# Kernel tuning notes

Measured on AMD Instinct MI355X. Metric: run time of the kernel, lower is better.

The kernel has to match this reference:

```python
import jax, jax.numpy as jnp
import numpy as np

OUT_H = OUT_W = 7
SCALE = 1.0 / 16.0
E = 256
HEADS = 8
DH = E // HEADS
ROI_GRID = 14          # scaled roi side (fixed by construction -> static shapes)
N_ROIS = 512
FH, FW = 152, 256
NQ = OUT_H * OUT_W     # 49 content queries
S = ROI_GRID * ROI_GRID  # 196 keys per roi


def setup_inputs() -> dict:
    key = jax.random.key(0)
    ks = jax.random.split(key, 8)
    features = jax.random.normal(ks[0], (1, E, FH, FW), jnp.float32)
    # rois [N,5] = (batch_idx, x1, y1, x2, y2) in image coords; side 224 px so
    # the rounded scaled grid is exactly 14x14 for every roi.
    side = ROI_GRID / SCALE  # 224.0
    x1 = jax.random.uniform(ks[1], (N_ROIS,), minval=0.0, maxval=FW / SCALE - side)
    y1 = jax.random.uniform(ks[2], (N_ROIS,), minval=0.0, maxval=FH / SCALE - side)
    rois = jnp.stack([jnp.zeros(N_ROIS), x1, y1, x1 + side, y1 + side], axis=1)
    content_queries = jax.random.normal(ks[3], (NQ, E), jnp.float32) * 0.02
    in_proj_weight = jax.random.normal(ks[4], (3 * E, E), jnp.float32) / np.sqrt(E)
    in_proj_bias = jnp.zeros((3 * E,), jnp.float32)
    out_proj_weight = jax.random.normal(ks[5], (E, E), jnp.float32) / np.sqrt(E)
    out_proj_bias = jnp.zeros((E,), jnp.float32)
    balance_param = jnp.asarray(0.0, jnp.float32)  # hardsigmoid -> 0.5
    return dict(features=features, rois=rois, content_queries=content_queries,
                in_proj_weight=in_proj_weight, in_proj_bias=in_proj_bias,
                out_proj_weight=out_proj_weight, out_proj_bias=out_proj_bias,
                balance_param=balance_param)


def _bilinear(fmap, y, x):
    """torchvision roi_align bilinear sampling. fmap [C,H,W]; y,x flat [S]."""
    C, H, W = fmap.shape
    valid = ((y >= -1.0) & (y <= H) & (x >= -1.0) & (x <= W)).astype(fmap.dtype)
    y = jnp.clip(y, 0.0, H - 1.0)
    x = jnp.clip(x, 0.0, W - 1.0)
    y0 = jnp.floor(y); x0 = jnp.floor(x)
    y0i = y0.astype(jnp.int32); x0i = x0.astype(jnp.int32)
    y1i = jnp.minimum(y0i + 1, H - 1); x1i = jnp.minimum(x0i + 1, W - 1)
    ly = y - y0; lx = x - x0; hy = 1.0 - ly; hx = 1.0 - lx
    f = lambda yi, xi: fmap[:, yi, xi]  # [C, S]
    val = (hy * hx) * f(y0i, x0i) + (hy * lx) * f(y0i, x1i) \
        + (ly * hx) * f(y1i, x0i) + (ly * lx) * f(y1i, x1i)
    return val * valid


def _roi_align(fmap, roi4, out_h, out_w, scale, sr):
    """aligned=True RoIAlign for one roi, static sampling ratio sr."""
    x1, y1, x2, y2 = roi4
    sx = x1 * scale - 0.5
    sy = y1 * scale - 0.5
    bw = (x2 - x1) * scale / out_w
    bh = (y2 - y1) * scale / out_h
    offs = (jnp.arange(sr, dtype=fmap.dtype) + 0.5) / sr
    ys = sy + (jnp.arange(out_h, dtype=fmap.dtype)[:, None] + offs[None, :]) * bh  # [out_h,sr]
    xs = sx + (jnp.arange(out_w, dtype=fmap.dtype)[:, None] + offs[None, :]) * bw  # [out_w,sr]
    Y = jnp.broadcast_to(ys[:, :, None, None], (out_h, sr, out_w, sr)).reshape(-1)
    X = jnp.broadcast_to(xs[None, None, :, :], (out_h, sr, out_w, sr)).reshape(-1)
    vals = _bilinear(fmap, Y, X)  # [C, out_h*sr*out_w*sr]
    C = fmap.shape[0]
    return vals.reshape(C, out_h, sr, out_w, sr).mean(axis=(2, 4))  # [C,out_h,out_w]


def reference(features, rois, content_queries, in_proj_weight, in_proj_bias,
              out_proj_weight, out_proj_bias, balance_param):
    fmap = features[0]                       # single image batch
    roi4 = rois[:, 1:]                       # boxes in image coords
    balance = jnp.clip(balance_param / 6.0 + 0.5, 0.0, 1.0)  # hardsigmoid(_balance)

    # position pool: RoIAlign(7x7, spatial_scale, sampling_ratio=-1 -> 2, aligned)
    pos = jax.vmap(lambda r: _roi_align(fmap, r, OUT_H, OUT_W, SCALE, 2))(roi4)
    pos = pos * balance                      # [N, C, 7, 7]

    # per-roi content pool on scaled rois at scale 1.0, grid 14x14, sr=1
    sroi = roi4 * SCALE
    cf = jax.vmap(lambda r: _roi_align(fmap, r, ROI_GRID, ROI_GRID, 1.0, 1))(sroi)
    cf = cf.reshape(N_ROIS, E, S).transpose(0, 2, 1)  # [N, S, E] (flatten(2).permute)

    # nn.MultiheadAttention(E, HEADS): shared queries, per-roi keys/values
    Wq, Wk, Wv = jnp.split(in_proj_weight, 3, axis=0)
    bq, bk, bv = jnp.split(in_proj_bias, 3, axis=0)
    q = (content_queries @ Wq.T + bq).reshape(NQ, HEADS, DH).transpose(1, 0, 2)  # [h,Q,d]
    k = (cf @ Wk.T + bk).reshape(N_ROIS, S, HEADS, DH)
    v = (cf @ Wv.T + bv).reshape(N_ROIS, S, HEADS, DH)
    logits = jnp.einsum('hqd,nshd->nhqs', q, k) / np.sqrt(DH).astype(np.float32)
    attn = jax.nn.softmax(logits, axis=-1)                     # [N,h,Q,S]
    o = jnp.einsum('nhqs,nshd->nqhd', attn, v).reshape(N_ROIS, NQ, E)
    o = o @ out_proj_weight.T + out_proj_bias                  # [N, Q, E]
    att = o.transpose(0, 2, 1).reshape(N_ROIS, E, OUT_H, OUT_W)  # .T.reshape per roi

    return pos + att * (1.0 - balance)
```

## Files before the change

kernel.cpp:

```cpp
#include <hip/hip_runtime.h>
#include <stdint.h>

#define E_DIM 256
#define HEADS 8
#define NQ 49
#define S_TOT 196
#define NROIS 512
#define FH 152
#define FW 256
#define HW_TOT (FH*FW)

typedef unsigned short u16;
typedef short bf16x8 __attribute__((ext_vector_type(8)));
typedef float f32x4 __attribute__((ext_vector_type(4)));
typedef unsigned short us8 __attribute__((ext_vector_type(8)));

#define MFMA(a,b,c) __builtin_amdgcn_mfma_f32_16x16x32_bf16((a),(b),(c),0,0,0)

__device__ __forceinline__ u16 f2bf(float f) {
  union { float f; uint32_t u; } v; v.f = f;
  uint32_t u = v.u;
  return (u16)((u + 0x7FFFu + ((u >> 16) & 1u)) >> 16);
}
__device__ __forceinline__ float bf2f(u16 h) {
  union { uint32_t u; float f; } v; v.u = ((uint32_t)h) << 16;
  return v.f;
}
__device__ __forceinline__ uint32_t cvtpk(float lo, float hi) {
  uint32_t r;
  asm("v_cvt_pk_bf16_f32 %0, %1, %2" : "=v"(r) : "v"(lo), "v"(hi));
  return r;
}
__device__ __forceinline__ bf16x8 ld_frag(const u16* p) {
  union { uint2 d[2]; bf16x8 v; } t;
  t.d[0] = *(const uint2*)(p);
  t.d[1] = *(const uint2*)(p + 4);
  return t.v;
}
__device__ __forceinline__ bf16x8 ld_frag_g(const u16* p) {
  union { uint4 d; bf16x8 v; } t;
  t.d = *(const uint4*)(p);
  return t.v;
}
__device__ __forceinline__ void gll16(const u16* g, u16* l) {
  __builtin_amdgcn_global_load_lds(
      (__attribute__((address_space(1))) void*)(g),
      (__attribute__((address_space(3))) void*)(l), 16, 0, 0);
}
__device__ __forceinline__ void win_stencil(const u16* win, int p00, int hf,
                                            float w00, float w01, float w10, float w11,
                                            float o[16]) {
  const int cA = ((hf << 1)*225) << 3;
  const int cB = cA + (225 << 3);
  const int q0 = p00 << 3;
  us8 a00 = *(const us8*)(win + cA + q0);
  us8 a01 = *(const us8*)(win + cA + q0 + 8);
  us8 a10 = *(const us8*)(win + cA + q0 + 120);
  us8 a11 = *(const us8*)(win + cA + q0 + 128);
  us8 b00 = *(const us8*)(win + cB + q0);
  us8 b01 = *(const us8*)(win + cB + q0 + 8);
  us8 b10 = *(const us8*)(win + cB + q0 + 120);
  us8 b11 = *(const us8*)(win + cB + q0 + 128);
#pragma unroll
  for (int c = 0; c < 8; ++c) {
    o[c]     = w00*bf2f(a00[c]) + w01*bf2f(a01[c]) + w10*bf2f(a10[c]) + w11*bf2f(a11[c]);
    o[c + 8] = w00*bf2f(b00[c]) + w01*bf2f(b01[c]) + w10*bf2f(b10[c]) + w11*bf2f(b11[c]);
  }
}

__global__ __launch_bounds__(256) void prep_small(
    const float* __restrict__ ipw, const float* __restrict__ opw,
    const float* __restrict__ ipb, const float* __restrict__ cq,
    u16* __restrict__ Wk, u16* __restrict__ Wv, u16* __restrict__ Wo,
    u16* __restrict__ qs)
{
  const int b = blockIdx.x;
  const int t = threadIdx.x;
  if (b < 256) {
    int i = (b << 8) + t;
    Wk[i] = f2bf(ipw[65536 + i]);
    Wv[i] = f2bf(ipw[131072 + i]);
    Wo[i] = f2bf(opw[i]);
  } else {
    const int idx = b - 256;
    const int h = idx >> 3;
    const int qq = ((idx & 7) << 3) + (t >> 5);
    const int d = t & 31;
    float acc = 0.f;
    if (qq < NQ) {
      const float4* wr = (const float4*)(ipw + (size_t)(h*32 + d)*256);
      const float4* cr = (const float4*)(cq + (size_t)qq*256);
      float s0 = 0.f, s1 = 0.f, s2 = 0.f, s3 = 0.f;
#pragma unroll
      for (int e = 0; e < 64; e += 4) {
        float4 a0 = cr[e],     b0 = wr[e];
        float4 a1 = cr[e + 1], b1 = wr[e + 1];
        float4 a2 = cr[e + 2], b2 = wr[e + 2];
        float4 a3 = cr[e + 3], b3 = wr[e + 3];
        s0 += a0.x*b0.x + a0.y*b0.y + a0.z*b0.z + a0.w*b0.w;
        s1 += a1.x*b1.x + a1.y*b1.y + a1.z*b1.z + a1.w*b1.w;
        s2 += a2.x*b2.x + a2.y*b2.y + a2.z*b2.z + a2.w*b2.w;
        s3 += a3.x*b3.x + a3.y*b3.y + a3.z*b3.z + a3.w*b3.w;
      }
      acc = (ipb[h*32 + d] + ((s0 + s1) + (s2 + s3))) * 0.17677669529663687f;
    }
    qs[h*2048 + qq*32 + d] = f2bf(acc);
  }
}

#define AT_ST 268
#define CT_ST 268
__global__ __launch_bounds__(512, 2) void proj_kv(
    const float* __restrict__ f, const u16* __restrict__ Wk, const u16* __restrict__ Wv,
    u16* __restrict__ fT, u16* __restrict__ fK, u16* __restrict__ fV)
{
  __shared__ union __align__(16) {
    u16 At[64][AT_ST];
    u16 ct[2][64][CT_ST];
  } sm;
  const int m0 = blockIdx.x << 6;
  const int t = threadIdx.x;
  const int lane = t & 63;
  const int w = t >> 6;
  const int g = lane >> 4, l15 = lane & 15;

  const int cp = t >> 4;
  const int hwq = (t & 15) << 2;
#pragma unroll
  for (int it = 0; it < 4; ++it) {
    int c = (it << 6) + (cp << 1);
    float4 v0 = *(const float4*)(f + (size_t)c*HW_TOT + m0 + hwq);
    float4 v1 = *(const float4*)(f + (size_t)(c + 1)*HW_TOT + m0 + hwq);
    *(uint32_t*)(&sm.At[hwq    ][c]) = cvtpk(v0.x, v1.x);
    *(uint32_t*)(&sm.At[hwq + 1][c]) = cvtpk(v0.y, v1.y);
    *(uint32_t*)(&sm.At[hwq + 2][c]) = cvtpk(v0.z, v1.z);
    *(uint32_t*)(&sm.At[hwq + 3][c]) = cvtpk(v0.w, v1.w);
  }
  __syncthreads();

  {
    int r = t >> 3, c0 = (t & 7) << 5;
    u16* dst = fT + (size_t)(m0 + r)*256 + c0;
#pragma unroll
    for (int k = 0; k < 4; ++k)
      *(us8*)(dst + (k << 3)) = *(const us8*)(&sm.At[r][c0 + (k << 3)]);
  }

  const int map = w >> 2;
  const u16* W = map ? Wv : Wk;
  const int nq = (w & 3) << 6;
  f32x4 acc[4][4];
#pragma unroll
  for (int mf = 0; mf < 4; ++mf)
#pragma unroll
    for (int nt = 0; nt < 4; ++nt) acc[mf][nt] = (f32x4){0.f,0.f,0.f,0.f};

#pragma unroll
  for (int kt = 0; kt < 8; ++kt) {
    bf16x8 a[4], bb[4];
#pragma unroll
    for (int mf = 0; mf < 4; ++mf)
      a[mf] = ld_frag(&sm.At[(mf << 4) + l15][(kt << 5) + (g << 3)]);
#pragma unroll
    for (int nt = 0; nt < 4; ++nt)
      bb[nt] = ld_frag_g(W + (size_t)(nq + (nt << 4) + l15)*256 + (kt << 5) + (g << 3));
#pragma unroll
    for (int mf = 0; mf < 4; ++mf)
#pragma unroll
      for (int nt = 0; nt < 4; ++nt)
        acc[mf][nt] = MFMA(a[mf], bb[nt], acc[mf][nt]);
  }
  __syncthreads();
#pragma unroll
  for (int mf = 0; mf < 4; ++mf)
#pragma unroll
    for (int nt = 0; nt < 4; ++nt)
#pragma unroll
      for (int i = 0; i < 4; ++i)
        sm.ct[map][(mf << 4) + (g << 2) + i][nq + (nt << 4) + l15] = f2bf(acc[mf][nt][i]);
  __syncthreads();
  const int map2 = w >> 2;
  u16* dstmap = map2 ? fV : fK;
#pragma unroll
  for (int hh = 0; hh < 2; ++hh) {
    int hsel = ((w & 3) << 1) + hh;
#pragma unroll
    for (int mi = 0; mi < 4; ++mi) {
      int m = (lane >> 2) + (mi << 4);
      int chunk = lane & 3;
      bf16x8 val = ld_frag(&sm.ct[map2][m][(hsel << 5) + (chunk << 3)]);
      u16* dst = dstmap + (((size_t)hsel*HW_TOT + m0 + m) << 5) + (chunk << 3);
      *(us8*)dst = *(const us8*)&val;
    }
  }
}

#define AT2_ST 228
#define KS_ST 36
#define VT_ST 228
#define OR_ST 36
#define AS_ST 260
#define PS_ST 260
struct SMemA {
  u16 attn[64][AT2_ST];
  u16 ksmp[208][KS_ST];
  u16 vT[32][VT_ST];
  u16 ore[64][OR_ST];
  u16 kwin[8192];
};
struct SMemC {
  u16 ast[NQ][AS_ST];
  u16 pos[NQ][PS_ST];
};
union __align__(16) SMem { SMemA a; SMemC c; };

__global__ __launch_bounds__(512, 4) void fused_roi_attn(
    const float* __restrict__ rois,
    const float* __restrict__ balance_p,
    const float* __restrict__ bv,
    const float* __restrict__ bout,
    const u16*  __restrict__ fT,
    const u16*  __restrict__ fK,
    const u16*  __restrict__ fV,
    const u16*  __restrict__ Woutbf,
    const u16*  __restrict__ qsPad,
    float* __restrict__ out)
{
  __shared__ SMem sm;
  u16* vwin = &sm.a.attn[0][0];
  const int tid = threadIdx.x;
  const int lane = tid & 63;
  const int w = tid >> 6;
  const int v = w >> 2;
  const int w2 = w & 3;
  const int g = lane >> 4;
  const int l15 = lane & 15;
  const int n = blockIdx.x;

  float X = rois[n*5 + 1] * 0.0625f;
  float Y = rois[n*5 + 2] * 0.0625f;
  float fx0 = floorf(X), fy0 = floorf(Y);
  const int ix0 = (int)fx0, iy0 = (int)fy0;
  const float lx = X - fx0, ly = Y - fy0;
  const float hx = 1.0f - lx, hy = 1.0f - ly;
  const float w00 = hy*hx, w01 = hy*lx, w10 = ly*hx, w11 = ly*lx;

  int srcoff[2];
#pragma unroll
  for (int i = 0; i < 2; ++i) {
    int u = (w << 7) + (i << 6) + lane;
    int uc = min(u, 899);
    int c = uc / 225;
    int p = uc - c*225;
    int pr = p / 15, pc2 = p - pr*15;
    int yg = min(iy0 + pr, FH - 1);
    int xg = min(ix0 + pc2, FW - 1);
    srcoff[i] = (((yg << 8) + xg) << 5) + (c << 3);
  }
  const int u0 = ((w << 7) << 3);
  const int u1 = u0 + (64 << 3);

  const int s_slot = tid & 255;
  const int hf = tid >> 8;
  const bool smp = s_slot < S_TOT;
  int p00 = 0;
  if (smp) { int gy = s_slot/14, gx = s_slot - gy*14; p00 = gy*15 + gx; }
  const int hstep = HW_TOT << 5;

  for (int i = tid; i < 32*32; i += 512) sm.a.vT[i >> 5][196 + (i & 31)] = 0;
  for (int i = tid; i < 64*16; i += 512) sm.a.attn[i >> 4][208 + (i & 15)] = 0;

  float bal;
  { float bp = balance_p[0]; bal = fminf(fmaxf(bp*(1.0f/6.0f) + 0.5f, 0.0f), 1.0f); }

  f32x4 attacc[8];
#pragma unroll
  for (int i = 0; i < 8; ++i) attacc[i] = (f32x4){0.f,0.f,0.f,0.f};

  gll16(fK + srcoff[0], sm.a.kwin + u0);
  gll16(fK + srcoff[1], sm.a.kwin + u1);

  for (int h = 0; h < HEADS; ++h) {
    __syncthreads();

    {
      const u16* fVh = fV + h*hstep;
      gll16(fVh + srcoff[0], vwin + u0);
      gll16(fVh + srcoff[1], vwin + u1);
    }
    if (smp) {
      float kk[16];
      win_stencil(sm.a.kwin, p00, hf, w00, w01, w10, w11, kk);
      u16* krow = &sm.a.ksmp[s_slot][hf << 4];
      uint2 q0 = {cvtpk(kk[0],kk[1]),   cvtpk(kk[2],kk[3])};
      uint2 q1 = {cvtpk(kk[4],kk[5]),   cvtpk(kk[6],kk[7])};
      uint2 q2 = {cvtpk(kk[8],kk[9]),   cvtpk(kk[10],kk[11])};
      uint2 q3 = {cvtpk(kk[12],kk[13]), cvtpk(kk[14],kk[15])};
      *(uint2*)(krow)      = q0;
      *(uint2*)(krow + 4)  = q1;
      *(uint2*)(krow + 8)  = q2;
      *(uint2*)(krow + 12) = q3;
    }
    __syncthreads();

    if (smp) {
      float vv[16];
      win_stencil(vwin, p00, hf, w00, w01, w10, w11, vv);
#pragma unroll
      for (int j = 0; j < 16; j += 2) {
        uint32_t p = cvtpk(vv[j], vv[j+1]);
        sm.a.vT[(hf << 4) + j][s_slot]     = (u16)p;
        sm.a.vT[(hf << 4) + j + 1][s_slot] = (u16)(p >> 16);
      }
    }
    __syncthreads();

    if (h + 1 < HEADS) {
      const u16* fKh = fK + (h+1)*hstep;
      gll16(fKh + srcoff[0], sm.a.kwin + u0);
      gll16(fKh + srcoff[1], sm.a.kwin + u1);
    }

    bf16x8 aq = ld_frag_g(qsPad + (size_t)((h << 6) + (w2 << 4) + l15)*32 + (g << 3));
    float sum[4] = {0.f, 0.f, 0.f, 0.f};
#pragma unroll
    for (int nt = 0; nt < 13; ++nt) {
      bf16x8 bk = ld_frag(&sm.a.ksmp[(nt << 4) + l15][g << 3]);
      f32x4 z = (f32x4){0.f,0.f,0.f,0.f};
      f32x4 lg = MFMA(aq, bk, z);
#pragma unroll
      for (int i = 0; i < 4; ++i) {
        float p = (nt == 12 && l15 >= 4) ? 0.f : __expf(fminf(lg[i], 80.f));
        sum[i] += p;
        sm.a.attn[(w2 << 4) + (g << 2) + i][(nt << 4) + l15] = f2bf(p);
      }
    }
    float srow[4];
#pragma unroll
    for (int i = 0; i < 4; ++i) {
#pragma unroll
      for (int off = 1; off < 16; off <<= 1) sum[i] += __shfl_xor(sum[i], off, 64);
      srow[i] = 1.0f / sum[i];
    }

    f32x4 o0 = (f32x4){0.f,0.f,0.f,0.f}, o1 = (f32x4){0.f,0.f,0.f,0.f};
#pragma unroll
    for (int kt = 0; kt < 7; ++kt) {
      bf16x8 ap = ld_frag(&sm.a.attn[(w2 << 4) + l15][(kt << 5) + (g << 3)]);
      bf16x8 b0 = ld_frag(&sm.a.vT[l15][(kt << 5) + (g << 3)]);
      bf16x8 b1 = ld_frag(&sm.a.vT[16 + l15][(kt << 5) + (g << 3)]);
      o0 = MFMA(ap, b0, o0);
      o1 = MFMA(ap, b1, o1);
    }
    float bv0 = bv[(h << 5) + l15];
    float bv1 = bv[(h << 5) + 16 + l15];
#pragma unroll
    for (int i = 0; i < 4; ++i) {
      sm.a.ore[(w2 << 4) + (g << 2) + i][l15]      = f2bf(o0[i]*srow[i] + bv0);
      sm.a.ore[(w2 << 4) + (g << 2) + i][16 + l15] = f2bf(o1[i]*srow[i] + bv1);
    }
    bf16x8 ao = ld_frag(&sm.a.ore[(w2 << 4) + l15][g << 3]);
#pragma unroll
    for (int j = 0; j < 8; ++j) {
      int nt = (v << 3) + j;
      bf16x8 bo = ld_frag_g(Woutbf + (size_t)((nt << 4) + l15)*256 + (h << 5) + (g << 3));
      attacc[j] = MFMA(ao, bo, attacc[j]);
    }
  }

  __syncthreads();
#pragma unroll
  for (int j = 0; j < 8; ++j) {
    int nt = (v << 3) + j;
    float bo = bout[(nt << 4) + l15];
#pragma unroll
    for (int i = 0; i < 4; ++i) {
      int r = (w2 << 4) + (g << 2) + i;
      if (r < NQ) sm.c.ast[r][(nt << 4) + l15] = f2bf(attacc[j][i] + bo);
    }
  }
  {
    float wy[3] = {hy, 1.0f, ly};
    float wx[3] = {hx, 1.0f, lx};
    for (int it = 0; it < 4; ++it) {
      int item = tid + (it << 9);
      if (item < NQ*32) {
        int q = item >> 5, c8 = (item & 31) << 3;
        int oy = q/7, ox = q - oy*7;
        float a[8] = {0.f,0.f,0.f,0.f,0.f,0.f,0.f,0.f};
#pragma unroll
        for (int j = 0; j < 3; ++j) {
          int ry = min(iy0 + (oy << 1) + j, FH - 1);
#pragma unroll
          for (int i = 0; i < 3; ++i) {
            int rx = min(ix0 + (ox << 1) + i, FW - 1);
            const u16* pt = fT + (((size_t)(ry*FW + rx)) << 8) + c8;
            us8 tv = *(const us8*)pt;
            float wji = wy[j]*wx[i];
#pragma unroll
            for (int c = 0; c < 8; ++c) a[c] += wji*bf2f(tv[c]);
          }
        }
        uint2 r0 = {cvtpk(0.25f*a[0], 0.25f*a[1]), cvtpk(0.25f*a[2], 0.25f*a[3])};
        uint2 r1 = {cvtpk(0.25f*a[4], 0.25f*a[5]), cvtpk(0.25f*a[6], 0.25f*a[7])};
        *(uint2*)(&sm.c.pos[q][c8])     = r0;
        *(uint2*)(&sm.c.pos[q][c8 + 4]) = r1;
      }
    }
  }
  __syncthreads();
  float ibal = 1.0f - bal;
  float* outp = out + (size_t)n*(E_DIM*NQ);
  for (int j = 0; j < 25; ++j) {
    int idx = (j << 9) + tid;
    if (idx < E_DIM*NQ) {
      int eo = idx/49;
      int q  = idx - eo*49;
      outp[idx] = bal*bf2f(sm.c.pos[q][eo]) + ibal*bf2f(sm.c.ast[q][eo]);
    }
  }
}

extern "C" void kernel_launch(void* const* d_in, const int* in_sizes, int n_in,
                              void* d_out, int out_size, void* d_ws, size_t ws_size,
                              hipStream_t stream) {
  const float* features = (const float*)d_in[0];
  const float* rois     = (const float*)d_in[1];
  const float* cq       = (const float*)d_in[2];
  const float* ipw      = (const float*)d_in[3];
  const float* ipb      = (const float*)d_in[4];
  const float* opw      = (const float*)d_in[5];
  const float* opb      = (const float*)d_in[6];
  const float* balp     = (const float*)d_in[7];
  float* out = (float*)d_out;

  char* ws = (char*)d_ws;
  const size_t FMB = (size_t)HW_TOT*256*2;
  u16* fT = (u16*)ws;
  u16* fK = (u16*)(ws + FMB);
  u16* fV = (u16*)(ws + 2*FMB);
  u16* Wk = (u16*)(ws + 3*FMB);
  u16* Wv = Wk + 65536;
  u16* Wo = Wv + 65536;
  u16* qs = Wo + 65536;

  hipLaunchKernelGGL(prep_small, dim3(320), dim3(256), 0, stream,
                     ipw, opw, ipb, cq, Wk, Wv, Wo, qs);
  hipLaunchKernelGGL(proj_kv,    dim3(HW_TOT/64), dim3(512), 0, stream,
                     features, Wk, Wv, fT, fK, fV);
  hipLaunchKernelGGL(fused_roi_attn, dim3(NROIS), dim3(512), 0, stream,
                     rois, balp, ipb + 512, opb, fT, fK, fV, Wo, qs, out);
}
```

Before: 136.5 us.

## Split feature transpose from K/V projection, pack bilinear math, use exp2 softmax

Moves the fp32-to-bf16 feature transpose into the prep kernel, handled by many small LDS-tiled blocks. The K/V projection becomes a separate smaller-tile GEMM that reads the transposed bf16 features from global memory. In the fused kernel, the bilinear stencil now works on packed float2 pairs, and the softmax uses exp2 with log2(e) folded into the query scale. The extra kernel boundary adds a round-trip of fT through global memory, and proj_gemm no longer shares its A tile through LDS.

```diff
diff --git a/kernel.cpp b/kernel.cpp
--- a/kernel.cpp
+++ b/kernel.cpp
@@ -13,7 +13,9 @@
 typedef unsigned short u16;
 typedef short bf16x8 __attribute__((ext_vector_type(8)));
 typedef float f32x4 __attribute__((ext_vector_type(4)));
+typedef float f32x2 __attribute__((ext_vector_type(2)));
 typedef unsigned short us8 __attribute__((ext_vector_type(8)));
+typedef unsigned int u32x4 __attribute__((ext_vector_type(4)));
 
 #define MFMA(a,b,c) __builtin_amdgcn_mfma_f32_16x16x32_bf16((a),(b),(c),0,0,0)
 
@@ -30,6 +32,11 @@
   uint32_t r;
   asm("v_cvt_pk_bf16_f32 %0, %1, %2" : "=v"(r) : "v"(lo), "v"(hi));
   return r;
+}
+__device__ __forceinline__ f32x2 bf2x2(uint32_t p) {
+  union { uint32_t u; float f; } lo, hi;
+  lo.u = p << 16; hi.u = p & 0xFFFF0000u;
+  return (f32x2){lo.f, hi.f};
 }
 __device__ __forceinline__ bf16x8 ld_frag(const u16* p) {
   union { uint2 d[2]; bf16x8 v; } t;
@@ -47,42 +54,64 @@
       (__attribute__((address_space(1))) void*)(g),
       (__attribute__((address_space(3))) void*)(l), 16, 0, 0);
 }
-__device__ __forceinline__ void win_stencil(const u16* win, int p00, int hf,
-                                            float w00, float w01, float w10, float w11,
-                                            float o[16]) {
+__device__ __forceinline__ void win_stencil2(const u16* win, int p00, int hf,
+                                             f32x2 W00, f32x2 W01, f32x2 W10, f32x2 W11,
+                                             f32x2 o[8]) {
   const int cA = ((hf << 1)*225) << 3;
   const int cB = cA + (225 << 3);
   const int q0 = p00 << 3;
-  us8 a00 = *(const us8*)(win + cA + q0);
-  us8 a01 = *(const us8*)(win + cA + q0 + 8);
-  us8 a10 = *(const us8*)(win + cA + q0 + 120);
-  us8 a11 = *(const us8*)(win + cA + q0 + 128);
-  us8 b00 = *(const us8*)(win + cB + q0);
-  us8 b01 = *(const us8*)(win + cB + q0 + 8);
-  us8 b10 = *(const us8*)(win + cB + q0 + 120);
-  us8 b11 = *(const us8*)(win + cB + q0 + 128);
-#pragma unroll
-  for (int c = 0; c < 8; ++c) {
-    o[c]     = w00*bf2f(a00[c]) + w01*bf2f(a01[c]) + w10*bf2f(a10[c]) + w11*bf2f(a11[c]);
-    o[c + 8] = w00*bf2f(b00[c]) + w01*bf2f(b01[c]) + w10*bf2f(b10[c]) + w11*bf2f(b11[c]);
-  }
-}
-
-__global__ __launch_bounds__(256) void prep_small(
-    const float* __restrict__ ipw, const float* __restrict__ opw,
-    const float* __restrict__ ipb, const float* __restrict__ cq,
-    u16* __restrict__ Wk, u16* __restrict__ Wv, u16* __restrict__ Wo,
-    u16* __restrict__ qs)
+  u32x4 a00 = *(const u32x4*)(win + cA + q0);
+  u32x4 a01 = *(const u32x4*)(win + cA + q0 + 8);
+  u32x4 a10 = *(const u32x4*)(win + cA + q0 + 120);
+  u32x4 a11 = *(const u32x4*)(win + cA + q0 + 128);
+  u32x4 b00 = *(const u32x4*)(win + cB + q0);
+  u32x4 b01 = *(const u32x4*)(win + cB + q0 + 8);
+  u32x4 b10 = *(const u32x4*)(win + cB + q0 + 120);
+  u32x4 b11 = *(const u32x4*)(win + cB + q0 + 128);
+#pragma unroll
+  for (int c = 0; c < 4; ++c) {
+    o[c]     = W00*bf2x2(a00[c]) + W01*bf2x2(a01[c]) + W10*bf2x2(a10[c]) + W11*bf2x2(a11[c]);
+    o[c + 4] = W00*bf2x2(b00[c]) + W01*bf2x2(b01[c]) + W10*bf2x2(b10[c]) + W11*bf2x2(b11[c]);
+  }
+}
+
+__global__ __launch_bounds__(256) void prep_trans(
+    const float* __restrict__ f, const float* __restrict__ ipw,
+    const float* __restrict__ opw, const float* __restrict__ ipb,
+    const float* __restrict__ cq,
+    u16* __restrict__ fT, u16* __restrict__ Wk, u16* __restrict__ Wv,
+    u16* __restrict__ Wo, u16* __restrict__ qs)
 {
   const int b = blockIdx.x;
   const int t = threadIdx.x;
-  if (b < 256) {
-    int i = (b << 8) + t;
+  if (b < 2432) {
+    __shared__ float tile[64][69];
+    const int hw0 = (b >> 2) << 6;
+    const int c0 = (b & 3) << 6;
+#pragma unroll
+    for (int i = 0; i < 4; ++i) {
+      int c_l = (t >> 4) + (i << 4);
+      int hw_l = (t & 15) << 2;
+      float4 v = *(const float4*)(f + (size_t)(c0 + c_l)*HW_TOT + hw0 + hw_l);
+      tile[c_l][hw_l] = v.x; tile[c_l][hw_l+1] = v.y;
+      tile[c_l][hw_l+2] = v.z; tile[c_l][hw_l+3] = v.w;
+    }
+    __syncthreads();
+    const int hw_l = t >> 2;
+    const int cc = (t & 3) << 4;
+    u16 tmp[16];
+#pragma unroll
+    for (int m = 0; m < 16; ++m) tmp[m] = f2bf(tile[cc + m][hw_l]);
+    u16* dst = fT + (size_t)(hw0 + hw_l)*256 + c0 + cc;
+    *(us8*)(dst)     = *(const us8*)(tmp);
+    *(us8*)(dst + 8) = *(const us8*)(tmp + 8);
+  } else if (b < 2688) {
+    int i = ((b - 2432) << 8) + t;
     Wk[i] = f2bf(ipw[65536 + i]);
     Wv[i] = f2bf(ipw[131072 + i]);
     Wo[i] = f2bf(opw[i]);
   } else {
-    const int idx = b - 256;
+    const int idx = b - 2688;
     const int h = idx >> 3;
     const int qq = ((idx & 7) << 3) + (t >> 5);
     const int d = t & 31;
@@ -102,96 +131,64 @@
         s2 += a2.x*b2.x + a2.y*b2.y + a2.z*b2.z + a2.w*b2.w;
         s3 += a3.x*b3.x + a3.y*b3.y + a3.z*b3.z + a3.w*b3.w;
       }
-      acc = (ipb[h*32 + d] + ((s0 + s1) + (s2 + s3))) * 0.17677669529663687f;
+      acc = (ipb[h*32 + d] + ((s0 + s1) + (s2 + s3))) * 0.25503487f;
     }
     qs[h*2048 + qq*32 + d] = f2bf(acc);
   }
 }
 
-#define AT_ST 268
 #define CT_ST 268
-__global__ __launch_bounds__(512, 2) void proj_kv(
-    const float* __restrict__ f, const u16* __restrict__ Wk, const u16* __restrict__ Wv,
-    u16* __restrict__ fT, u16* __restrict__ fK, u16* __restrict__ fV)
+__global__ __launch_bounds__(256, 4) void proj_gemm(
+    const u16* __restrict__ fT, const u16* __restrict__ Wk, const u16* __restrict__ Wv,
+    u16* __restrict__ fK, u16* __restrict__ fV)
 {
-  __shared__ union __align__(16) {
-    u16 At[64][AT_ST];
-    u16 ct[2][64][CT_ST];
-  } sm;
-  const int m0 = blockIdx.x << 6;
+  __shared__ u16 ct[2][32][CT_ST];
+  const int m0 = blockIdx.x << 5;
   const int t = threadIdx.x;
   const int lane = t & 63;
   const int w = t >> 6;
   const int g = lane >> 4, l15 = lane & 15;
-
-  const int cp = t >> 4;
-  const int hwq = (t & 15) << 2;
-#pragma unroll
-  for (int it = 0; it < 4; ++it) {
-    int c = (it << 6) + (cp << 1);
-    float4 v0 = *(const float4*)(f + (size_t)c*HW_TOT + m0 + hwq);
-    float4 v1 = *(const float4*)(f + (size_t)(c + 1)*HW_TOT + m0 + hwq);
-    *(uint32_t*)(&sm.At[hwq    ][c]) = cvtpk(v0.x, v1.x);
-    *(uint32_t*)(&sm.At[hwq + 1][c]) = cvtpk(v0.y, v1.y);
-    *(uint32_t*)(&sm.At[hwq + 2][c]) = cvtpk(v0.z, v1.z);
-    *(uint32_t*)(&sm.At[hwq + 3][c]) = cvtpk(v0.w, v1.w);
-  }
+  const int map = w >> 1;
+  const int nh = w & 1;
+  const u16* W = map ? Wv : Wk;
+
+  f32x4 acc[2][8];
+#pragma unroll
+  for (int mf = 0; mf < 2; ++mf)
+#pragma unroll
+    for (int nt = 0; nt < 8; ++nt) acc[mf][nt] = (f32x4){0.f,0.f,0.f,0.f};
+
+#pragma unroll
+  for (int kt = 0; kt < 8; ++kt) {
+    bf16x8 a0 = ld_frag_g(fT + (size_t)(m0 + l15)*256 + (kt << 5) + (g << 3));
+    bf16x8 a1 = ld_frag_g(fT + (size_t)(m0 + 16 + l15)*256 + (kt << 5) + (g << 3));
+#pragma unroll
+    for (int nt = 0; nt < 8; ++nt) {
+      bf16x8 bb = ld_frag_g(W + (size_t)((nh << 7) + (nt << 4) + l15)*256 + (kt << 5) + (g << 3));
+      acc[0][nt] = MFMA(a0, bb, acc[0][nt]);
+      acc[1][nt] = MFMA(a1, bb, acc[1][nt]);
+    }
+  }
+#pragma unroll
+  for (int mf = 0; mf < 2; ++mf)
+#pragma unroll
+    for (int nt = 0; nt < 8; ++nt)
+#pragma unroll
+      for (int i = 0; i < 4; ++i)
+        ct[map][(mf << 4) + (g << 2) + i][(nh << 7) + (nt << 4) + l15] = f2bf(acc[mf][nt][i]);
   __syncthreads();
-
-  {
-    int r = t >> 3, c0 = (t & 7) << 5;
-    u16* dst = fT + (size_t)(m0 + r)*256 + c0;
-#pragma unroll
-    for (int k = 0; k < 4; ++k)
-      *(us8*)(dst + (k << 3)) = *(const us8*)(&sm.At[r][c0 + (k << 3)]);
-  }
-
-  const int map = w >> 2;
-  const u16* W = map ? Wv : Wk;
-  const int nq = (w & 3) << 6;
-  f32x4 acc[4][4];
-#pragma unroll
-  for (int mf = 0; mf < 4; ++mf)
-#pragma unroll
-    for (int nt = 0; nt < 4; ++nt) acc[mf][nt] = (f32x4){0.f,0.f,0.f,0.f};
-
-#pragma unroll
-  for (int kt = 0; kt < 8; ++kt) {
-    bf16x8 a[4], bb[4];
-#pragma unroll
-    for (int mf = 0; mf < 4; ++mf)
-      a[mf] = ld_frag(&sm.At[(mf << 4) + l15][(kt << 5) + (g << 3)]);
-#pragma unroll
-    for (int nt = 0; nt < 4; ++nt)
-      bb[nt] = ld_frag_g(W + (size_t)(nq + (nt << 4) + l15)*256 + (kt << 5) + (g << 3));
-#pragma unroll
-    for (int mf = 0; mf < 4; ++mf)
-#pragma unroll
-      for (int nt = 0; nt < 4; ++nt)
-        acc[mf][nt] = MFMA(a[mf], bb[nt], acc[mf][nt]);
-  }
-  __syncthreads();
-#pragma unroll
-  for (int mf = 0; mf < 4; ++mf)
-#pragma unroll
-    for (int nt = 0; nt < 4; ++nt)
-#pragma unroll
-      for (int i = 0; i < 4; ++i)
-        sm.ct[map][(mf << 4) + (g << 2) + i][nq + (nt << 4) + l15] = f2bf(acc[mf][nt][i]);
-  __syncthreads();
-  const int map2 = w >> 2;
+  const int map2 = t >> 7;
+  const int r2 = (t >> 2) & 31;
+  const int hq = t & 3;
   u16* dstmap = map2 ? fV : fK;
 #pragma unroll
-  for (int hh = 0; hh < 2; ++hh) {
-    int hsel = ((w & 3) << 1) + hh;
-#pragma unroll
-    for (int mi = 0; mi < 4; ++mi) {
-      int m = (lane >> 2) + (mi << 4);
-      int chunk = lane & 3;
-      bf16x8 val = ld_frag(&sm.ct[map2][m][(hsel << 5) + (chunk << 3)]);
-      u16* dst = dstmap + (((size_t)hsel*HW_TOT + m0 + m) << 5) + (chunk << 3);
-      *(us8*)dst = *(const us8*)&val;
-    }
+  for (int e = 0; e < 2; ++e) {
+    int hsel = (hq << 1) + e;
+    u16* dst = dstmap + (((size_t)hsel*HW_TOT + m0 + r2) << 5);
+    const u16* srcp = &ct[map2][r2][hsel << 5];
+#pragma unroll
+    for (int chunk = 0; chunk < 4; ++chunk)
+      *(us8*)(dst + (chunk << 3)) = *(const us8*)(srcp + (chunk << 3));
   }
 }
 
@@ -244,6 +241,7 @@
   const float lx = X - fx0, ly = Y - fy0;
   const float hx = 1.0f - lx, hy = 1.0f - ly;
   const float w00 = hy*hx, w01 = hy*lx, w10 = ly*hx, w11 = ly*lx;
+  const f32x2 W00 = {w00, w00}, W01 = {w01, w01}, W10 = {w10, w10}, W11 = {w11, w11};
 
   int srcoff[2];
 #pragma unroll
@@ -289,13 +287,13 @@
       gll16(fVh + srcoff[1], vwin + u1);
     }
     if (smp) {
-      float kk[16];
-      win_stencil(sm.a.kwin, p00, hf, w00, w01, w10, w11, kk);
+      f32x2 kk[8];
+      win_stencil2(sm.a.kwin, p00, hf, W00, W01, W10, W11, kk);
       u16* krow = &sm.a.ksmp[s_slot][hf << 4];
-      uint2 q0 = {cvtpk(kk[0],kk[1]),   cvtpk(kk[2],kk[3])};
-      uint2 q1 = {cvtpk(kk[4],kk[5]),   cvtpk(kk[6],kk[7])};
-      uint2 q2 = {cvtpk(kk[8],kk[9]),   cvtpk(kk[10],kk[11])};
-      uint2 q3 = {cvtpk(kk[12],kk[13]), cvtpk(kk[14],kk[15])};
+      uint2 q0 = {cvtpk(kk[0].x,kk[0].y), cvtpk(kk[1].x,kk[1].y)};
+      uint2 q1 = {cvtpk(kk[2].x,kk[2].y), cvtpk(kk[3].x,kk[3].y)};
+      uint2 q2 = {cvtpk(kk[4].x,kk[4].y), cvtpk(kk[5].x,kk[5].y)};
+      uint2 q3 = {cvtpk(kk[6].x,kk[6].y), cvtpk(kk[7].x,kk[7].y)};
       *(uint2*)(krow)      = q0;
       *(uint2*)(krow + 4)  = q1;
       *(uint2*)(krow + 8)  = q2;
@@ -304,13 +302,13 @@
     __syncthreads();
 
     if (smp) {
-      float vv[16];
-      win_stencil(vwin, p00, hf, w00, w01, w10, w11, vv);
-#pragma unroll
-      for (int j = 0; j < 16; j += 2) {
-        uint32_t p = cvtpk(vv[j], vv[j+1]);
-        sm.a.vT[(hf << 4) + j][s_slot]     = (u16)p;
-        sm.a.vT[(hf << 4) + j + 1][s_slot] = (u16)(p >> 16);
+      f32x2 vv[8];
+      win_stencil2(vwin, p00, hf, W00, W01, W10, W11, vv);
+#pragma unroll
+      for (int jp = 0; jp < 8; ++jp) {
+        uint32_t p = cvtpk(vv[jp].x, vv[jp].y);
+        sm.a.vT[(hf << 4) + 2*jp][s_slot]     = (u16)p;
+        sm.a.vT[(hf << 4) + 2*jp + 1][s_slot] = (u16)(p >> 16);
       }
     }
     __syncthreads();
@@ -330,9 +328,10 @@
       f32x4 lg = MFMA(aq, bk, z);
 #pragma unroll
       for (int i = 0; i < 4; ++i) {
-        float p = (nt == 12 && l15 >= 4) ? 0.f : __expf(fminf(lg[i], 80.f));
+        float p = (nt == 12 && l15 >= 4) ? 0.f
+                  : __builtin_amdgcn_exp2f(fminf(lg[i], 115.f));
         sum[i] += p;
-        sm.a.attn[(w2 << 4) + (g << 2) + i][(nt << 4) + l15] = f2bf(p);
+        sm.a.attn[(w2 << 4) + (g << 2) + i][(nt << 4) + l15] = (u16)cvtpk(p, p);
       }
     }
     float srow[4];
@@ -444,10 +443,10 @@
   u16* Wo = Wv + 65536;
   u16* qs = Wo + 65536;
 
-  hipLaunchKernelGGL(prep_small, dim3(320), dim3(256), 0, stream,
-                     ipw, opw, ipb, cq, Wk, Wv, Wo, qs);
-  hipLaunchKernelGGL(proj_kv,    dim3(HW_TOT/64), dim3(512), 0, stream,
-                     features, Wk, Wv, fT, fK, fV);
+  hipLaunchKernelGGL(prep_trans, dim3(2752), dim3(256), 0, stream,
+                     features, ipw, opw, ipb, cq, fT, Wk, Wv, Wo, qs);
+  hipLaunchKernelGGL(proj_gemm,  dim3(HW_TOT/32), dim3(256), 0, stream,
+                     fT, Wk, Wv, fK, fV);
   hipLaunchKernelGGL(fused_roi_attn, dim3(NROIS), dim3(512), 0, stream,
                      rois, balp, ipb + 512, opb, fT, fK, fV, Wo, qs, out);
 }
```

New measurement: 171.2 us. 1.25x slower.
